# Kernel optimization log

Hardware: AMD Instinct MI355X
Metric: run time of the kernel (lower is better)

Reference implementation:

```python
import jax, jax.numpy as jnp
import numpy as np

B, D, H, C = 8192, 1024, 4, 4  # batch, input_dim, num_heads, num_classes


def setup_inputs() -> dict:
    key = jax.random.key(0)
    ks = jax.random.split(key, 24)
    s = 0.02
    n = jax.random.normal
    d = {
        "X1": n(ks[0], (B, D), jnp.float32),
        "X2": n(ks[1], (B, D), jnp.float32),
        "X3": n(ks[2], (B, D), jnp.float32),
        "X4": n(ks[3], (B, D), jnp.float32),
        # shared Q projection (injected into both self- and cross-attn at init)
        "Wq": n(ks[4], (D, D), jnp.float32) * s,
        "bq": jnp.zeros((D,), jnp.float32),
        # self-attention K/V/out projections
        "Wk_s": n(ks[5], (D, D), jnp.float32) * s,
        "bk_s": jnp.zeros((D,), jnp.float32),
        "Wv_s": n(ks[6], (D, D), jnp.float32) * s,
        "bv_s": jnp.zeros((D,), jnp.float32),
        "Wo_s": n(ks[7], (D, D), jnp.float32) * s,
        "bo_s": jnp.zeros((D,), jnp.float32),
        # cross-attention K/V/out projections
        "Wk_c": n(ks[8], (D, D), jnp.float32) * s,
        "bk_c": jnp.zeros((D,), jnp.float32),
        "Wv_c": n(ks[9], (D, D), jnp.float32) * s,
        "bv_c": jnp.zeros((D,), jnp.float32),
        "Wo_c": n(ks[10], (D, D), jnp.float32) * s,
        "bo_c": jnp.zeros((D,), jnp.float32),
        # classifier
        "Wc": n(ks[11], (C, D), jnp.float32) * s,
        "bc": jnp.zeros((C,), jnp.float32),
    }
    return d


def _mha(q, kv, Wq, bq, Wk, bk, Wv, bv, Wo, bo):
    # q: (B, Lq, D), kv: (B, Lk, D); matches torch nn.MultiheadAttention math
    Bq, Lq, Dm = q.shape
    Lk = kv.shape[1]
    hd = Dm // H
    Q = (q @ Wq.T + bq).reshape(Bq, Lq, H, hd).transpose(0, 2, 1, 3)
    K = (kv @ Wk.T + bk).reshape(Bq, Lk, H, hd).transpose(0, 2, 1, 3)
    V = (kv @ Wv.T + bv).reshape(Bq, Lk, H, hd).transpose(0, 2, 1, 3)
    scores = jnp.einsum('bhqd,bhkd->bhqk', Q, K) / jnp.sqrt(jnp.float32(hd))
    attn = jax.nn.softmax(scores, axis=-1)
    out = jnp.einsum('bhqk,bhkd->bhqd', attn, V)
    out = out.transpose(0, 2, 1, 3).reshape(Bq, Lq, Dm)
    return out @ Wo.T + bo


def _diff_attn(query, key_list, p):
    # query: (B, D); key_list: list of 3 (B, D)
    q1 = query[:, None, :]  # (B, 1, D)
    self_out = _mha(q1, q1, p['Wq'], p['bq'], p['Wk_s'], p['bk_s'],
                    p['Wv_s'], p['bv_s'], p['Wo_s'], p['bo_s'])
    keys = jnp.stack(key_list, axis=1)          # (B, 3, D)
    differ_keys = q1 - keys                      # (B, 3, D)
    cross_out = _mha(q1, differ_keys, p['Wq'], p['bq'], p['Wk_c'], p['bk_c'],
                     p['Wv_c'], p['bv_c'], p['Wo_c'], p['bo_c'])
    return (self_out + cross_out)[:, 0]          # (B, D)


def reference(X1, X2, X3, X4, Wq, bq, Wk_s, bk_s, Wv_s, bv_s, Wo_s, bo_s,
              Wk_c, bk_c, Wv_c, bv_c, Wo_c, bo_c, Wc, bc):
    p = dict(Wq=Wq, bq=bq, Wk_s=Wk_s, bk_s=bk_s, Wv_s=Wv_s, bv_s=bv_s,
             Wo_s=Wo_s, bo_s=bo_s, Wk_c=Wk_c, bk_c=bk_c, Wv_c=Wv_c,
             bv_c=bv_c, Wo_c=Wo_c, bo_c=bo_c)
    d1 = _diff_attn(X1, [X2, X3, X4], p)
    d2 = _diff_attn(X2, [X1, X3, X4], p)
    d3 = _diff_attn(X3, [X1, X2, X4], p)
    d4 = _diff_attn(X4, [X1, X2, X3], p)
    features = jnp.concatenate([d1, d2, d3, d4], axis=0)  # (4B, D)
    logits = features @ Wc.T + bc                          # (4B, C)
    return (d1, d2, d3, d4, logits)
```

## Files before the change

### kernel.cpp

```cpp
#include <hip/hip_runtime.h>

typedef __bf16 bf16x8 __attribute__((ext_vector_type(8)));
typedef float f32x4 __attribute__((ext_vector_type(4)));

__device__ __forceinline__ float bf2f(unsigned short u) {
  union { unsigned int i; float f; } c; c.i = ((unsigned int)u) << 16; return c.f;
}
__device__ __forceinline__ unsigned short f2bf(float f) {
  union { float f; unsigned int i; } c; c.f = f;
  unsigned int u = c.i;
  u += 0x7FFFu + ((u >> 16) & 1u);
  return (unsigned short)(u >> 16);
}

#define GLDS16(g, l)                                                          \
  __builtin_amdgcn_global_load_lds(                                           \
      (const __attribute__((address_space(1))) void*)(g),                     \
      (__attribute__((address_space(3))) void*)(l), 16, 0, 0)

#define MFMA16(a, b, c) __builtin_amdgcn_mfma_f32_16x16x32_bf16(a, b, c, 0, 0, 0)


__global__ __launch_bounds__(256) void convert_x(
    const float* __restrict__ X1, const float* __restrict__ X2,
    const float* __restrict__ X3, const float* __restrict__ X4,
    unsigned short* __restrict__ Xcat)
{
  int gid = blockIdx.x * 256 + threadIdx.x;
  size_t base = (size_t)gid * 4;
  int sec = (int)(base >> 23);
  int off = (int)(base & 8388607);
  const float* s = sec == 0 ? X1 : sec == 1 ? X2 : sec == 2 ? X3 : X4;
  float4 v = *(const float4*)(s + off);
  ushort4 o;
  o.x = f2bf(v.x); o.y = f2bf(v.y); o.z = f2bf(v.z); o.w = f2bf(v.w);
  *(ushort4*)(Xcat + base) = o;
}

__global__ __launch_bounds__(256) void prep_w(
    const float* __restrict__ Wq,  const float* __restrict__ Wk_c,
    const float* __restrict__ Wv_c, const float* __restrict__ Wo_c,
    const float* __restrict__ Wo_s,
    unsigned short* __restrict__ Wcat, unsigned short* __restrict__ WoM2,
    unsigned short* __restrict__ Wos_bf)
{
  int gid = blockIdx.x * 256 + threadIdx.x;
  if (gid < 786432) {
    int base = gid * 4;
    int sec = base >> 20, off = base & 1048575;
    const float* s = sec == 0 ? Wk_c : sec == 1 ? Wv_c : Wq;
    float4 v = *(const float4*)(s + off);
    ushort4 o;
    o.x = f2bf(v.x); o.y = f2bf(v.y); o.z = f2bf(v.z); o.w = f2bf(v.w);
    *(ushort4*)(Wcat + base) = o;
  } else if (gid < 1048576) {
    int idx = (gid - 786432) * 4;
    int n = idx >> 10, c = idx & 1023;
    float4 v = *(const float4*)(Wo_c + (size_t)n * 1024 + c);
    ushort4 o;
    o.x = f2bf(v.x); o.y = f2bf(v.y); o.z = f2bf(v.z); o.w = f2bf(v.w);
    *(ushort4*)(WoM2 + (size_t)n * 2048 + c) = o;
  } else if (gid < 1310720) {
    int base = (gid - 1048576) * 4;
    float4 v = *(const float4*)(Wo_s + base);
    ushort4 o;
    o.x = f2bf(v.x); o.y = f2bf(v.y); o.z = f2bf(v.z); o.w = f2bf(v.w);
    *(ushort4*)(Wos_bf + base) = o;
  }
}

__global__ __launch_bounds__(256) void transpose_wvs(
    const float* __restrict__ Wv_s, unsigned short* __restrict__ WvsT)
{
  __shared__ float tile[32][33];
  const int r = threadIdx.x >> 3;
  const int c4 = (threadIdx.x & 7) * 4;
  const int j0 = blockIdx.y * 32, k0 = blockIdx.x * 32;
  float4 v = *(const float4*)(Wv_s + (size_t)(j0 + r) * 1024 + k0 + c4);
  tile[r][c4] = v.x; tile[r][c4 + 1] = v.y; tile[r][c4 + 2] = v.z; tile[r][c4 + 3] = v.w;
  __syncthreads();
  ushort4 o;
  o.x = f2bf(tile[c4 + 0][r]); o.y = f2bf(tile[c4 + 1][r]);
  o.z = f2bf(tile[c4 + 2][r]); o.w = f2bf(tile[c4 + 3][r]);
  *(ushort4*)(WvsT + (size_t)(k0 + r) * 1024 + j0 + c4) = o;
}

__global__ __launch_bounds__(256) void bias2_kernel(
    const float* __restrict__ Wo_s, const float* __restrict__ bv_s,
    const float* __restrict__ bo_c, const float* __restrict__ bo_s,
    float* __restrict__ bias2)
{
  const int wv = threadIdx.x >> 6, l = threadIdx.x & 63;
  const int n = blockIdx.x * 4 + wv;
  const float* row = Wo_s + (size_t)n * 1024;
  float s = 0.f;
#pragma unroll
  for (int it = 0; it < 4; ++it) {
    int j = it * 256 + l * 4;
    float4 w = *(const float4*)(row + j);
    float4 b = *(const float4*)(bv_s + j);
    s += w.x * b.x + w.y * b.y + w.z * b.z + w.w * b.w;
  }
#pragma unroll
  for (int d = 1; d < 64; d <<= 1) s += __shfl_xor(s, d);
  if (l == 0) bias2[n] = s + bo_c[n] + bo_s[n];
}

template<bool OUT_F32, bool HAS_BIAS>
__global__ __launch_bounds__(256) void gemm_bt(
    const unsigned short* __restrict__ A1, int lda1, int K1,
    const unsigned short* __restrict__ A2, int lda2, int K2,
    const unsigned short* __restrict__ Bw, int ldb,
    void* __restrict__ Cout, int ldc,
    const float* __restrict__ bias)
{
  __shared__ char lds[16384];
  char* ldsA = lds;
  char* ldsB = lds + 8192;

  const int t = threadIdx.x;
  const int l = t & 63;
  const int wv = t >> 6;
  const int wr = wv >> 1, wc = wv & 1;
  const int bM = blockIdx.y * 128, bN = blockIdx.x * 128;

  const int pa0 = t, pa1 = t + 256;
  const int ra0 = pa0 >> 2, ra1 = pa1 >> 2;
  const int ca0 = (((pa0 & 3) ^ ((ra0 >> 1) & 3))) * 8;
  const int ca1 = (((pa1 & 3) ^ ((ra1 >> 1) & 3))) * 8;
  const unsigned short* gB0 = Bw + (size_t)(bN + ra0) * ldb + ca0;
  const unsigned short* gB1 = Bw + (size_t)(bN + ra1) * ldb + ca1;
  char* lA0 = ldsA + pa0 * 16; char* lA1 = ldsA + pa1 * 16;
  char* lB0 = ldsB + pa0 * 16; char* lB1 = ldsB + pa1 * 16;

  const int rA = wr * 64 + (l & 15);
  const int rB = wc * 64 + (l & 15);
  const int cA = ((l >> 4) ^ ((rA >> 1) & 3)) * 16;
  const int cB = ((l >> 4) ^ ((rB >> 1) & 3)) * 16;
  const char* fA = ldsA + rA * 64 + cA;
  const char* fB = ldsB + rB * 64 + cB;

  f32x4 acc[4][4] = {};

  const unsigned short* gA0 = A1 + (size_t)(bM + ra0) * lda1 + ca0;
  const unsigned short* gA1 = A1 + (size_t)(bM + ra1) * lda1 + ca1;

  for (int src = 0; src < 2; ++src) {
    const int Kc = src ? K2 : K1;
    if (src) {
      if (K2 == 0) break;
      gA0 = A2 + (size_t)(bM + ra0) * lda2 + ca0;
      gA1 = A2 + (size_t)(bM + ra1) * lda2 + ca1;
    }
    for (int k0 = 0; k0 < Kc; k0 += 32) {
      GLDS16(gA0, lA0); GLDS16(gA1, lA1);
      GLDS16(gB0, lB0); GLDS16(gB1, lB1);
      gA0 += 32; gA1 += 32; gB0 += 32; gB1 += 32;
      __syncthreads();

      bf16x8 af[4], bfv[4];
#pragma unroll
      for (int i = 0; i < 4; ++i) af[i] = *(const bf16x8*)(fA + i * 1024);
#pragma unroll
      for (int i = 0; i < 4; ++i) bfv[i] = *(const bf16x8*)(fB + i * 1024);
#pragma unroll
      for (int mt = 0; mt < 4; ++mt)
#pragma unroll
        for (int nt = 0; nt < 4; ++nt)
          acc[mt][nt] = MFMA16(af[mt], bfv[nt], acc[mt][nt]);
      __syncthreads();
    }
  }

  const int mrow = bM + wr * 64 + ((l >> 4) << 2);
  const int ncol = bN + wc * 64 + (l & 15);
  float bvals[4];
  if (HAS_BIAS) {
#pragma unroll
    for (int nt = 0; nt < 4; ++nt) bvals[nt] = bias[ncol + nt * 16];
  }
#pragma unroll
  for (int mt = 0; mt < 4; ++mt)
#pragma unroll
    for (int nt = 0; nt < 4; ++nt)
#pragma unroll
      for (int r = 0; r < 4; ++r) {
        size_t idx = (size_t)(mrow + mt * 16 + r) * ldc + (ncol + nt * 16);
        float v = acc[mt][nt][r];
        if (HAS_BIAS) v += bvals[nt];
        if (OUT_F32) ((float*)Cout)[idx] = v;
        else         ((unsigned short*)Cout)[idx] = f2bf(v);
      }
}

template<bool OUT_F32, bool HAS_BIAS>
__global__ __launch_bounds__(512, 2) void gemm256(
    const unsigned short* __restrict__ A1, int lda1, int K1,
    const unsigned short* __restrict__ A2, int lda2, int K2,
    const unsigned short* __restrict__ Bw, int ldb,
    void* __restrict__ Cout, int ldc,
    const float* __restrict__ bias)
{
  __shared__ __align__(128) char lds[131072];

  const int tid = threadIdx.x;
  const int l  = tid & 63;
  const int wv = tid >> 6;
  const int wr = wv >> 2, wc = wv & 3;

  const int nN = gridDim.x;
  int lin = blockIdx.y * nN + blockIdx.x;
  int nwg = nN * gridDim.y;
  int id2 = ((nwg & 7) == 0) ? ((lin & 7) * (nwg >> 3) + (lin >> 3)) : lin;
  const int bM = (id2 / nN) * 256;
  const int bN = (id2 % nN) * 256;

  const int NT1 = K1 >> 6;
  const int NT  = (K1 + K2) >> 6;

  const int sr0  = tid >> 2;
  const int colE = ((tid & 3) ^ ((sr0 >> 1) & 3)) * 8;
  const unsigned short* pA1g0 = A1 + (size_t)(bM + sr0) * lda1 + colE;
  const unsigned short* pA1g1 = A1 + (size_t)(bM + sr0 + 128) * lda1 + colE;
  const unsigned short* pA2g0 = (K2 > 0) ? A2 + (size_t)(bM + sr0) * lda2 + colE : pA1g0;
  const unsigned short* pA2g1 = (K2 > 0) ? A2 + (size_t)(bM + sr0 + 128) * lda2 + colE : pA1g1;
  const unsigned short* pBg0  = Bw + (size_t)(bN + sr0) * ldb + colE;
  const unsigned short* pBg1  = Bw + (size_t)(bN + sr0 + 128) * ldb + colE;
  char* ldsw = lds + tid * 16;

  auto stageA = [&](int tt, int kh) {
    const unsigned short *p0, *p1; int tc;
    if (tt < NT1) { p0 = pA1g0; p1 = pA1g1; tc = (tt << 6) + (kh << 5); }
    else          { p0 = pA2g0; p1 = pA2g1; tc = ((tt - NT1) << 6) + (kh << 5); }
    unsigned off = (unsigned)((tt & 1) << 16) + (unsigned)(kh << 14);
    GLDS16(p0 + tc, ldsw + off);
    GLDS16(p1 + tc, ldsw + off + 8192);
  };
  auto stageB = [&](int tt, int kh) {
    int tc = (tt << 6) + (kh << 5);
    unsigned off = (unsigned)((tt & 1) << 16) + 32768u + (unsigned)(kh << 14);
    GLDS16(pBg0 + tc, ldsw + off);
    GLDS16(pBg1 + tc, ldsw + off + 8192);
  };

  const int swz = ((l >> 4) ^ (((l & 15) >> 1) & 3)) << 4;
  const char* rdA0 = lds + ((wr * 128 + (l & 15)) * 64 + swz);
  const char* rdB0 = lds + (32768 + (wc * 64 + (l & 15)) * 64 + swz);

  f32x4 acc[8][4] = {};

  stageA(0, 0); stageB(0, 0); stageA(0, 1); stageB(0, 1);
  stageA(1, 0); stageB(1, 0); stageA(1, 1);
  asm volatile("s_waitcnt vmcnt(10)" ::: "memory");
  __builtin_amdgcn_s_barrier();

  for (int t = 0; t < NT; ++t) {
    const char* rA = rdA0 + ((t & 1) << 16);
    const char* rB = rdB0 + ((t & 1) << 16);
    bf16x8 af[8], bfr[4];

#pragma unroll
    for (int m = 0; m < 8; ++m) af[m] = *(const bf16x8*)(rA + m * 1024);
#pragma unroll
    for (int n = 0; n < 4; ++n) bfr[n] = *(const bf16x8*)(rB + n * 1024);
    if (t + 1 < NT) stageB(t + 1, 1);
    __builtin_amdgcn_s_barrier();
    asm volatile("s_waitcnt lgkmcnt(0)" ::: "memory");
    __builtin_amdgcn_s_setprio(1);
#pragma unroll
    for (int m = 0; m < 8; ++m) {
      acc[m][0] = MFMA16(af[m], bfr[0], acc[m][0]);
      acc[m][1] = MFMA16(af[m], bfr[1], acc[m][1]);
    }
    __builtin_amdgcn_s_setprio(0);
    __builtin_amdgcn_s_barrier();

    if (t + 2 < NT) stageA(t + 2, 0);
    if (t < NT - 2)       asm volatile("s_waitcnt vmcnt(6)" ::: "memory");
    else if (t == NT - 2) asm volatile("s_waitcnt vmcnt(4)" ::: "memory");
    else                  asm volatile("s_waitcnt vmcnt(0)" ::: "memory");
    __builtin_amdgcn_s_barrier();
    __builtin_amdgcn_s_setprio(1);
#pragma unroll
    for (int m = 0; m < 8; ++m) {
      acc[m][2] = MFMA16(af[m], bfr[2], acc[m][2]);
      acc[m][3] = MFMA16(af[m], bfr[3], acc[m][3]);
    }
    __builtin_amdgcn_s_setprio(0);
    __builtin_amdgcn_s_barrier();

#pragma unroll
    for (int m = 0; m < 8; ++m) af[m] = *(const bf16x8*)(rA + 16384 + m * 1024);
#pragma unroll
    for (int n = 0; n < 4; ++n) bfr[n] = *(const bf16x8*)(rB + 16384 + n * 1024);
    if (t + 2 < NT) stageB(t + 2, 0);
    __builtin_amdgcn_s_barrier();
    asm volatile("s_waitcnt lgkmcnt(0)" ::: "memory");
    __builtin_amdgcn_s_setprio(1);
#pragma unroll
    for (int m = 0; m < 8; ++m) {
      acc[m][0] = MFMA16(af[m], bfr[0], acc[m][0]);
      acc[m][1] = MFMA16(af[m], bfr[1], acc[m][1]);
    }
    __builtin_amdgcn_s_setprio(0);
    __builtin_amdgcn_s_barrier();

    if (t + 2 < NT) stageA(t + 2, 1);
    __builtin_amdgcn_s_barrier();
    __builtin_amdgcn_s_setprio(1);
#pragma unroll
    for (int m = 0; m < 8; ++m) {
      acc[m][2] = MFMA16(af[m], bfr[2], acc[m][2]);
      acc[m][3] = MFMA16(af[m], bfr[3], acc[m][3]);
    }
    __builtin_amdgcn_s_setprio(0);
    __builtin_amdgcn_s_barrier();
  }

  const int mb = bM + wr * 128 + ((l >> 4) << 2);
  const int nb = bN + wc * 64 + (l & 15);
  float bvals[4];
  if (HAS_BIAS) {
#pragma unroll
    for (int n = 0; n < 4; ++n) bvals[n] = bias[nb + n * 16];
  }
#pragma unroll
  for (int m = 0; m < 8; ++m)
#pragma unroll
    for (int n = 0; n < 4; ++n)
#pragma unroll
      for (int r = 0; r < 4; ++r) {
        size_t idx = (size_t)(mb + m * 16 + r) * ldc + (nb + n * 16);
        float v = acc[m][n][r];
        if (HAS_BIAS) v += bvals[n];
        if (OUT_F32) ((float*)Cout)[idx] = v;
        else         ((unsigned short*)Cout)[idx] = f2bf(v);
      }
}

__global__ __launch_bounds__(256) void attn_kernel(
    unsigned short* __restrict__ Yp,
    const float* __restrict__ bq,  const float* __restrict__ bkc,
    const float* __restrict__ bvc)
{
  const int b = blockIdx.x;
  const int h = threadIdx.x >> 6;
  const int l = threadIdx.x & 63;
  const int e0 = h * 256 + l * 4;

  const float4 bqv = *(const float4*)(bq + e0);
  const float4 bkv = *(const float4*)(bkc + e0);
  const float4 bvv = *(const float4*)(bvc + e0);

  float q[4][4], kc[4][4], vc[4][4];
  size_t rb[4];
#pragma unroll
  for (int i = 0; i < 4; ++i) {
    rb[i] = ((size_t)i * 8192 + b) * 3072;
    ushort4 qq = *(const ushort4*)(Yp + rb[i] + 2048 + e0);
    ushort4 kk = *(const ushort4*)(Yp + rb[i] + e0);
    ushort4 vv = *(const ushort4*)(Yp + rb[i] + 1024 + e0);
    q[i][0] = bf2f(qq.x) + bqv.x; q[i][1] = bf2f(qq.y) + bqv.y;
    q[i][2] = bf2f(qq.z) + bqv.z; q[i][3] = bf2f(qq.w) + bqv.w;
    kc[i][0] = bf2f(kk.x); kc[i][1] = bf2f(kk.y);
    kc[i][2] = bf2f(kk.z); kc[i][3] = bf2f(kk.w);
    vc[i][0] = bf2f(vv.x); vc[i][1] = bf2f(vv.y);
    vc[i][2] = bf2f(vv.z); vc[i][3] = bf2f(vv.w);
  }

  float u[4][4], tb[4];
#pragma unroll
  for (int i = 0; i < 4; ++i) {
    tb[i] = q[i][0]*bkv.x + q[i][1]*bkv.y + q[i][2]*bkv.z + q[i][3]*bkv.w;
#pragma unroll
    for (int j = 0; j < 4; ++j)
      u[i][j] = q[i][0]*kc[j][0] + q[i][1]*kc[j][1] + q[i][2]*kc[j][2] + q[i][3]*kc[j][3];
  }
#pragma unroll
  for (int d = 1; d < 64; d <<= 1) {
#pragma unroll
    for (int i = 0; i < 4; ++i) {
      tb[i] += __shfl_xor(tb[i], d);
#pragma unroll
      for (int j = 0; j < 4; ++j) u[i][j] += __shfl_xor(u[i][j], d);
    }
  }

#pragma unroll
  for (int i = 0; i < 4; ++i) {
    float s[4], a[4];
    float mx = -1e30f;
#pragma unroll
    for (int j = 0; j < 4; ++j) {
      s[j] = (u[i][i] - u[i][j] + tb[i]) * 0.0625f;
      if (j != i) mx = fmaxf(mx, s[j]);
    }
    float den = 0.f;
#pragma unroll
    for (int j = 0; j < 4; ++j) {
      a[j] = (j == i) ? 0.f : __expf(s[j] - mx);
      den += a[j];
    }
    float inv = 1.f / den;
#pragma unroll
    for (int j = 0; j < 4; ++j) a[j] *= inv;

    float o0 = vc[i][0] + bvv.x, o1 = vc[i][1] + bvv.y;
    float o2 = vc[i][2] + bvv.z, o3 = vc[i][3] + bvv.w;
#pragma unroll
    for (int j = 0; j < 4; ++j) {
      o0 -= a[j] * vc[j][0]; o1 -= a[j] * vc[j][1];
      o2 -= a[j] * vc[j][2]; o3 -= a[j] * vc[j][3];
    }
    ushort4 w;
    w.x = f2bf(o0); w.y = f2bf(o1); w.z = f2bf(o2); w.w = f2bf(o3);
    *(ushort4*)(Yp + rb[i] + 2048 + e0) = w;
  }
}

__global__ __launch_bounds__(256) void logits_kernel(
    const float* __restrict__ feats, const float* __restrict__ Wc,
    const float* __restrict__ bc, float* __restrict__ out)
{
  __shared__ float w[4096];
  const int t = threadIdx.x;
  for (int i = t; i < 4096; i += 256) w[i] = Wc[i];
  __syncthreads();
  const int wave = t >> 6, l = t & 63;
  const int row = blockIdx.x * 4 + wave;
  const float* f = feats + (size_t)row * 1024;
  float s0 = 0.f, s1 = 0.f, s2 = 0.f, s3 = 0.f;
#pragma unroll
  for (int c4 = 0; c4 < 4; ++c4) {
    int e = c4 * 256 + l * 4;
    float4 x  = *(const float4*)(f + e);
    float4 w0 = *(const float4*)(w + e);
    float4 w1 = *(const float4*)(w + 1024 + e);
    float4 w2 = *(const float4*)(w + 2048 + e);
    float4 w3 = *(const float4*)(w + 3072 + e);
    s0 += x.x*w0.x + x.y*w0.y + x.z*w0.z + x.w*w0.w;
    s1 += x.x*w1.x + x.y*w1.y + x.z*w1.z + x.w*w1.w;
    s2 += x.x*w2.x + x.y*w2.y + x.z*w2.z + x.w*w2.w;
    s3 += x.x*w3.x + x.y*w3.y + x.z*w3.z + x.w*w3.w;
  }
#pragma unroll
  for (int d = 1; d < 64; d <<= 1) {
    s0 += __shfl_xor(s0, d); s1 += __shfl_xor(s1, d);
    s2 += __shfl_xor(s2, d); s3 += __shfl_xor(s3, d);
  }
  if (l < 4) {
    float s = (l == 0) ? s0 : (l == 1) ? s1 : (l == 2) ? s2 : s3;
    out[(size_t)row * 4 + l] = s + bc[l];
  }
}

extern "C" void kernel_launch(void* const* d_in, const int* in_sizes, int n_in,
                              void* d_out, int out_size, void* d_ws, size_t ws_size,
                              hipStream_t stream) {
  const float* X1   = (const float*)d_in[0];
  const float* X2   = (const float*)d_in[1];
  const float* X3   = (const float*)d_in[2];
  const float* X4   = (const float*)d_in[3];
  const float* Wq   = (const float*)d_in[4];
  const float* bq   = (const float*)d_in[5];
  const float* Wv_s = (const float*)d_in[8];
  const float* bv_s = (const float*)d_in[9];
  const float* Wo_s = (const float*)d_in[10];
  const float* bo_s = (const float*)d_in[11];
  const float* Wk_c = (const float*)d_in[12];
  const float* bk_c = (const float*)d_in[13];
  const float* Wv_c = (const float*)d_in[14];
  const float* bv_c = (const float*)d_in[15];
  const float* Wo_c = (const float*)d_in[16];
  const float* bo_c = (const float*)d_in[17];
  const float* Wc   = (const float*)d_in[18];
  const float* bc   = (const float*)d_in[19];

  char* ws = (char*)d_ws;
  unsigned short* Xcat   = (unsigned short*)(ws + 0);
  unsigned short* Wcat   = (unsigned short*)(ws + 67108864);
  unsigned short* WoM2   = (unsigned short*)(ws + 73400320);
  unsigned short* Wos_bf = (unsigned short*)(ws + 77594624);
  unsigned short* WvsT   = (unsigned short*)(ws + 79691776);
  float*          bias2  = (float*)        (ws + 81788928);
  unsigned short* Yproj  = (unsigned short*)(ws + 81793024);
  float* out = (float*)d_out;

  convert_x<<<32768, 256, 0, stream>>>(X1, X2, X3, X4, Xcat);
  prep_w<<<5120, 256, 0, stream>>>(Wq, Wk_c, Wv_c, Wo_c, Wo_s, Wcat, WoM2, Wos_bf);
  transpose_wvs<<<dim3(32, 32), 256, 0, stream>>>(Wv_s, WvsT);
  bias2_kernel<<<256, 256, 0, stream>>>(Wo_s, bv_s, bo_c, bo_s, bias2);
  gemm_bt<false, false><<<dim3(8, 8), 256, 0, stream>>>(
      Wos_bf, 1024, 1024, nullptr, 0, 0, WvsT, 1024,
      (void*)(WoM2 + 1024), 2048, nullptr);
  gemm256<false, false><<<dim3(12, 128), 512, 0, stream>>>(
      Xcat, 1024, 1024, nullptr, 0, 0, Wcat, 1024,
      (void*)Yproj, 3072, nullptr);
  attn_kernel<<<8192, 256, 0, stream>>>(Yproj, bq, bk_c, bv_c);
  gemm256<true, true><<<dim3(4, 128), 512, 0, stream>>>(
      Yproj + 2048, 3072, 1024, Xcat, 1024, 1024, WoM2, 2048,
      (void*)out, 1024, bias2);
  logits_kernel<<<8192, 256, 0, stream>>>(out, Wc, bc, out + 33554432);
}
```

Baseline: 725.5 us.

## Stage GEMM epilogue through LDS for vector stores and trim main-loop barriers

The GEMM epilogue used to write each accumulator element straight to global memory as a scalar, strided store. It now writes the tile into swizzled LDS first, then copies it out with coalesced 16-byte row stores, in two halves for fp32 output. The main loop is also reordered: B fragments are read around the A fragment loads, several barriers and explicit lgkmcnt waits are removed, and the vmcnt thresholds are adjusted so global prefetch overlaps more MFMA work. The goal is to cut store transaction overhead and synchronisation stalls. The cost is extra LDS traffic and __syncthreads in the epilogue, plus a risk of LDS hazards now that fewer barriers guard the buffer reuse.

After: 710.7 us. 1.02x faster.

```diff
diff --git a/kernel.cpp b/kernel.cpp
--- a/kernel.cpp
+++ b/kernel.cpp
@@ -259,13 +259,13 @@
     const char* rB = rdB0 + ((t & 1) << 16);
     bf16x8 af[8], bfr[4];
 
+    bfr[0] = *(const bf16x8*)(rB);
+    bfr[1] = *(const bf16x8*)(rB + 1024);
 #pragma unroll
     for (int m = 0; m < 8; ++m) af[m] = *(const bf16x8*)(rA + m * 1024);
-#pragma unroll
-    for (int n = 0; n < 4; ++n) bfr[n] = *(const bf16x8*)(rB + n * 1024);
+    bfr[2] = *(const bf16x8*)(rB + 2048);
+    bfr[3] = *(const bf16x8*)(rB + 3072);
     if (t + 1 < NT) stageB(t + 1, 1);
-    __builtin_amdgcn_s_barrier();
-    asm volatile("s_waitcnt lgkmcnt(0)" ::: "memory");
     __builtin_amdgcn_s_setprio(1);
 #pragma unroll
     for (int m = 0; m < 8; ++m) {
@@ -276,66 +276,112 @@
     __builtin_amdgcn_s_barrier();
 
     if (t + 2 < NT) stageA(t + 2, 0);
-    if (t < NT - 2)       asm volatile("s_waitcnt vmcnt(6)" ::: "memory");
+    __builtin_amdgcn_s_setprio(1);
+#pragma unroll
+    for (int m = 0; m < 8; ++m) {
+      acc[m][2] = MFMA16(af[m], bfr[2], acc[m][2]);
+      acc[m][3] = MFMA16(af[m], bfr[3], acc[m][3]);
+    }
+    __builtin_amdgcn_s_setprio(0);
+    if (t < NT - 2)       asm volatile("s_waitcnt vmcnt(10)" ::: "memory");
+    else if (t == NT - 2) asm volatile("s_waitcnt vmcnt(8)" ::: "memory");
+    else                  asm volatile("s_waitcnt vmcnt(0)" ::: "memory");
+    __builtin_amdgcn_s_barrier();
+
+    bfr[0] = *(const bf16x8*)(rB + 16384);
+    bfr[1] = *(const bf16x8*)(rB + 16384 + 1024);
+#pragma unroll
+    for (int m = 0; m < 8; ++m) af[m] = *(const bf16x8*)(rA + 16384 + m * 1024);
+    bfr[2] = *(const bf16x8*)(rB + 16384 + 2048);
+    bfr[3] = *(const bf16x8*)(rB + 16384 + 3072);
+    if (t + 2 < NT) stageB(t + 2, 0);
+    __builtin_amdgcn_s_setprio(1);
+#pragma unroll
+    for (int m = 0; m < 8; ++m) {
+      acc[m][0] = MFMA16(af[m], bfr[0], acc[m][0]);
+      acc[m][1] = MFMA16(af[m], bfr[1], acc[m][1]);
+    }
+    __builtin_amdgcn_s_setprio(0);
+    __builtin_amdgcn_s_barrier();
+
+    if (t + 2 < NT) stageA(t + 2, 1);
+    __builtin_amdgcn_s_setprio(1);
+#pragma unroll
+    for (int m = 0; m < 8; ++m) {
+      acc[m][2] = MFMA16(af[m], bfr[2], acc[m][2]);
+      acc[m][3] = MFMA16(af[m], bfr[3], acc[m][3]);
+    }
+    __builtin_amdgcn_s_setprio(0);
+    if (t < NT - 2)       asm volatile("s_waitcnt vmcnt(10)" ::: "memory");
     else if (t == NT - 2) asm volatile("s_waitcnt vmcnt(4)" ::: "memory");
     else                  asm volatile("s_waitcnt vmcnt(0)" ::: "memory");
     __builtin_amdgcn_s_barrier();
-    __builtin_amdgcn_s_setprio(1);
-#pragma unroll
-    for (int m = 0; m < 8; ++m) {
-      acc[m][2] = MFMA16(af[m], bfr[2], acc[m][2]);
-      acc[m][3] = MFMA16(af[m], bfr[3], acc[m][3]);
-    }
-    __builtin_amdgcn_s_setprio(0);
-    __builtin_amdgcn_s_barrier();
-
-#pragma unroll
-    for (int m = 0; m < 8; ++m) af[m] = *(const bf16x8*)(rA + 16384 + m * 1024);
-#pragma unroll
-    for (int n = 0; n < 4; ++n) bfr[n] = *(const bf16x8*)(rB + 16384 + n * 1024);
-    if (t + 2 < NT) stageB(t + 2, 0);
-    __builtin_amdgcn_s_barrier();
-    asm volatile("s_waitcnt lgkmcnt(0)" ::: "memory");
-    __builtin_amdgcn_s_setprio(1);
-#pragma unroll
-    for (int m = 0; m < 8; ++m) {
-      acc[m][0] = MFMA16(af[m], bfr[0], acc[m][0]);
-      acc[m][1] = MFMA16(af[m], bfr[1], acc[m][1]);
-    }
-    __builtin_amdgcn_s_setprio(0);
-    __builtin_amdgcn_s_barrier();
-
-    if (t + 2 < NT) stageA(t + 2, 1);
-    __builtin_amdgcn_s_barrier();
-    __builtin_amdgcn_s_setprio(1);
-#pragma unroll
-    for (int m = 0; m < 8; ++m) {
-      acc[m][2] = MFMA16(af[m], bfr[2], acc[m][2]);
-      acc[m][3] = MFMA16(af[m], bfr[3], acc[m][3]);
-    }
-    __builtin_amdgcn_s_setprio(0);
-    __builtin_amdgcn_s_barrier();
-  }
-
-  const int mb = bM + wr * 128 + ((l >> 4) << 2);
-  const int nb = bN + wc * 64 + (l & 15);
+  }
+
+  const int lr0 = wr * 128 + ((l >> 4) << 2);
+  const int lc0 = wc * 64 + (l & 15);
   float bvals[4];
   if (HAS_BIAS) {
 #pragma unroll
-    for (int n = 0; n < 4; ++n) bvals[n] = bias[nb + n * 16];
-  }
-#pragma unroll
-  for (int m = 0; m < 8; ++m)
-#pragma unroll
-    for (int n = 0; n < 4; ++n)
-#pragma unroll
-      for (int r = 0; r < 4; ++r) {
-        size_t idx = (size_t)(mb + m * 16 + r) * ldc + (nb + n * 16);
-        float v = acc[m][n][r];
-        if (HAS_BIAS) v += bvals[n];
-        if (OUT_F32) ((float*)Cout)[idx] = v;
-        else         ((unsigned short*)Cout)[idx] = f2bf(v);
+    for (int n = 0; n < 4; ++n) bvals[n] = bias[bN + lc0 + n * 16];
+  }
+
+  if (!OUT_F32) {
+    unsigned short* lt = (unsigned short*)lds;
+    unsigned short* Cp = (unsigned short*)Cout;
+#pragma unroll
+    for (int m = 0; m < 8; ++m)
+#pragma unroll
+      for (int n = 0; n < 4; ++n)
+#pragma unroll
+        for (int r = 0; r < 4; ++r) {
+          float v = acc[m][n][r];
+          if (HAS_BIAS) v += bvals[n];
+          int row = lr0 + m * 16 + r;
+          int col = lc0 + n * 16;
+          int a = row * 256 + ((((col >> 3) ^ ((row >> 2) & 3)) << 3) | (col & 7));
+          lt[a] = f2bf(v);
+        }
+    __syncthreads();
+#pragma unroll
+    for (int i = 0; i < 16; ++i) {
+      int ch = i * 512 + tid;
+      int row = ch >> 5, c = ch & 31;
+      uint4 v = *(const uint4*)(lt + row * 256 + ((c ^ ((row >> 2) & 3)) << 3));
+      *(uint4*)(Cp + (size_t)(bM + row) * ldc + bN + c * 8) = v;
+    }
+  } else {
+    float* lf = (float*)lds;
+    float* Cp = (float*)Cout;
+#pragma unroll
+    for (int h = 0; h < 2; ++h) {
+      if (wr == h) {
+        const int lrh = (l >> 4) << 2;
+#pragma unroll
+        for (int m = 0; m < 8; ++m)
+#pragma unroll
+          for (int n = 0; n < 4; ++n)
+#pragma unroll
+            for (int r = 0; r < 4; ++r) {
+              float v = acc[m][n][r];
+              if (HAS_BIAS) v += bvals[n];
+              int row = lrh + m * 16 + r;
+              int col = lc0 + n * 16;
+              int a = row * 256 + ((((col >> 2) ^ ((row >> 2) & 3)) << 2) | (col & 3));
+              lf[a] = v;
+            }
       }
+      __syncthreads();
+#pragma unroll
+      for (int i = 0; i < 16; ++i) {
+        int ch = i * 512 + tid;
+        int row = ch >> 6, c = ch & 63;
+        float4 v = *(const float4*)(lf + row * 256 + ((c ^ ((row >> 2) & 3)) << 2));
+        *(float4*)(Cp + (size_t)(bM + h * 128 + row) * ldc + bN + c * 4) = v;
+      }
+      __syncthreads();
+    }
+  }
 }
 
 __global__ __launch_bounds__(256) void attn_kernel(
```
